# Kernel tuning notes

Measured on AMD Instinct MI355X. Metric: run time of the kernel, lower is better.

## Reference

```python
import jax, jax.numpy as jnp
import numpy as np

DIM = 64  # per-head dim; temperature init = sqrt(DIM)
B, H, S, D = 4, 12, 2048, 64


def setup_inputs() -> dict:
    key = jax.random.key(0)
    kq, kk, kv = jax.random.split(key, 3)
    Q = jax.random.normal(kq, (B, H, S, D), dtype=jnp.float32)
    K = jax.random.normal(kk, (B, H, S, D), dtype=jnp.float32)
    V = jax.random.normal(kv, (B, H, S, D), dtype=jnp.float32)
    temperature = jnp.ones((1,), dtype=jnp.float32) * (DIM ** 0.5)
    return {"Q": Q, "K": K, "V": V, "temperature": temperature}


def reference(Q, K, V, temperature):
    # scores: [B,H,S,S]
    scores = jnp.einsum("bhqd,bhkd->bhqk", Q, K) / temperature
    s = scores.shape[-1]
    eye = jnp.eye(s, dtype=bool)  # diagonal self-exclusion
    scores = jnp.where(eye, -jnp.inf, scores)
    attn = jax.nn.softmax(scores, axis=-1)
    return jnp.einsum("bhqk,bhkd->bhqd", attn, V)
```

## Files before the change

kernel.cpp:

```cpp
#include <hip/hip_runtime.h>
#include <hip/hip_bf16.h>

#define S_LEN 2048
#define D_DIM 64
#define NHEADS 48
#define QT 128
#define KT 64
#define NKT (S_LEN / KT)
#define HEAD_ELEMS ((size_t)S_LEN * D_DIM)
#define WS_NEED (3ull * NHEADS * S_LEN * D_DIM * 2ull)

typedef short bf16x8 __attribute__((ext_vector_type(8)));
typedef float f32x4 __attribute__((ext_vector_type(4)));

__device__ __forceinline__ unsigned short f2bf(float x) {
    unsigned u = __builtin_bit_cast(unsigned, x);
    u = (u + 0x7fffu + ((u >> 16) & 1u)) >> 16;
    return (unsigned short)u;
}

__device__ __forceinline__ unsigned cvtpk(float lo, float hi) {
    unsigned r;
    asm("v_cvt_pk_bf16_f32 %0, %1, %2" : "=v"(r) : "v"(lo), "v"(hi));
    return r;
}

__device__ __forceinline__ void gload16(const void* g, void* l) {
    __builtin_amdgcn_global_load_lds(
        (const __attribute__((address_space(1))) unsigned int*)g,
        (__attribute__((address_space(3))) unsigned int*)l, 16, 0, 0);
}

__global__ __launch_bounds__(256) void lsa_prep(
    const float* __restrict__ Qg, const float* __restrict__ Kg,
    const float* __restrict__ Vg, const float* __restrict__ Tg,
    unsigned short* __restrict__ Qs, unsigned short* __restrict__ Kf,
    unsigned short* __restrict__ Vf) {
    const int b   = blockIdx.x;
    const int tid = threadIdx.x;
    const int r   = tid >> 4;
    const int c4  = (tid & 15) * 4;

    __shared__ __align__(16) unsigned short Kl[4096];
    __shared__ __align__(16) unsigned short Vl[4096];

    const size_t ibase = (size_t)b * 4096;
    const float qscale = 1.442695041f / Tg[0];

#pragma unroll
    for (int it = 0; it < 4; ++it) {
        const int rr = it * 16 + r;
        const size_t off = ibase + (size_t)rr * D_DIM + c4;

        float4 q4 = *(const float4*)(Qg + off);
        uint2 qo;
        qo.x = cvtpk(q4.x * qscale, q4.y * qscale);
        qo.y = cvtpk(q4.z * qscale, q4.w * qscale);
        *(uint2*)&Qs[off] = qo;

        float4 k4 = *(const float4*)(Kg + off);
        {
            const int f = rr >> 4, l15 = rr & 15;
            const int c = c4 >> 5, lhi = (c4 >> 3) & 3, j0 = c4 & 7;
            uint2 ko;
            ko.x = cvtpk(k4.x, k4.y);
            ko.y = cvtpk(k4.z, k4.w);
            *(uint2*)&Kl[c * 2048 + f * 512 + ((lhi << 4) | l15) * 8 + j0] = ko;
        }

        float4 v4 = *(const float4*)(Vg + off);
        {
            const int cc = rr >> 5, rem = rr & 31;
            const int jv = ((rem >> 4) << 2) | (rem & 3);
            const int lhiv = (rem >> 2) & 3;
            const int g = c4 >> 4;
            const int base = cc * 2048 + g * 512 + (lhiv << 7) + jv;
            Vl[base + ((c4 + 0) & 15) * 8] = f2bf(v4.x);
            Vl[base + ((c4 + 1) & 15) * 8] = f2bf(v4.y);
            Vl[base + ((c4 + 2) & 15) * 8] = f2bf(v4.z);
            Vl[base + ((c4 + 3) & 15) * 8] = f2bf(v4.w);
        }
    }
    __syncthreads();
    const uint4* ks = (const uint4*)Kl;
    const uint4* vs = (const uint4*)Vl;
    uint4* kd = (uint4*)(Kf + ibase);
    uint4* vd = (uint4*)(Vf + ibase);
    kd[tid]       = ks[tid];
    kd[tid + 256] = ks[tid + 256];
    vd[tid]       = vs[tid];
    vd[tid + 256] = vs[tid + 256];
}

__global__ __launch_bounds__(256, 2) void lsa_attn_lds(
    const unsigned short* __restrict__ Qs, const unsigned short* __restrict__ Kf,
    const unsigned short* __restrict__ Vf, float* __restrict__ Og) {

    const int bid  = blockIdx.x;
    const int xcd  = bid & 7;
    const int idx  = bid >> 3;
    const int bh   = xcd * 6 + (idx >> 4);
    const int qt   = idx & 15;
    const int tid  = threadIdx.x;
    const int wid  = tid >> 6;
    const int lane = tid & 63;
    const int l15  = lane & 15;
    const int lhi  = lane >> 4;

    __shared__ __align__(16) unsigned short KV[2][2][KT * D_DIM];

    const unsigned short* Qh = Qs + (size_t)bh * HEAD_ELEMS;
    const char* Kh = (const char*)(Kf + (size_t)bh * HEAD_ELEMS);
    const char* Vh = (const char*)(Vf + (size_t)bh * HEAD_ELEMS);
    float* Ob = Og + (size_t)bh * HEAD_ELEMS;

    const int qbase   = qt * QT + wid * 32;
    const int diag_kt = qbase >> 6;

    bf16x8 qf[2][2];
#pragma unroll
    for (int rb = 0; rb < 2; ++rb) {
#pragma unroll
        for (int c = 0; c < 2; ++c) {
            qf[rb][c] = *(const bf16x8*)(Qh + (size_t)(qbase + rb * 16 + l15) * D_DIM
                                            + c * 32 + lhi * 8);
        }
    }

    const f32x4 zero4 = {0.f, 0.f, 0.f, 0.f};
    f32x4 acc[2][4];
    float mrow[2], lp[2];
#pragma unroll
    for (int rb = 0; rb < 2; ++rb) {
#pragma unroll
        for (int g = 0; g < 4; ++g) acc[rb][g] = zero4;
        mrow[rb] = -1e30f; lp[rb] = 0.f;
    }

    bf16x8 vr[8];
    f32x4 sf[2][4];
    bf16x8 pb[2][2];

#define ISSUE(BUF, T) do {                                                     \
    const char* ks_ = Kh + (size_t)(T) * 8192 + wid * 2048;                    \
    const char* vs_ = Vh + (size_t)(T) * 8192 + wid * 2048;                    \
    char* lk_ = (char*)&KV[BUF][0][0] + wid * 2048;                            \
    char* lv_ = (char*)&KV[BUF][1][0] + wid * 2048;                            \
    gload16(ks_ + lane * 16, lk_);                                             \
    gload16(ks_ + 1024 + lane * 16, lk_ + 1024);                               \
    gload16(vs_ + lane * 16, lv_);                                             \
    gload16(vs_ + 1024 + lane * 16, lv_ + 1024);                               \
} while (0)

#define DSQK(BUF) do {                                                         \
    const char* lk_ = (const char*)&KV[BUF][0][0] + lane * 16;                 \
    _Pragma("unroll")                                                          \
    for (int rb = 0; rb < 2; ++rb) {                                           \
        _Pragma("unroll")                                                      \
        for (int f = 0; f < 4; ++f) sf[rb][f] = zero4;                         \
    }                                                                          \
    _Pragma("unroll")                                                          \
    for (int c = 0; c < 2; ++c) {                                              \
        bf16x8 kb_[4];                                                         \
        _Pragma("unroll")                                                      \
        for (int f = 0; f < 4; ++f) {                                          \
            kb_[f] = *(const bf16x8*)(lk_ + c * 4096 + f * 1024);              \
        }                                                                      \
        __builtin_amdgcn_s_setprio(1);                                         \
        _Pragma("unroll")                                                      \
        for (int rb = 0; rb < 2; ++rb) {                                       \
            _Pragma("unroll")                                                  \
            for (int f = 0; f < 4; ++f) {                                      \
                sf[rb][f] = __builtin_amdgcn_mfma_f32_16x16x32_bf16(           \
                    kb_[f], qf[rb][c], sf[rb][f], 0, 0, 0);                    \
            }                                                                  \
        }                                                                      \
        __builtin_amdgcn_s_setprio(0);                                         \
    }                                                                          \
} while (0)

#define DSV(BUF) do {                                                          \
    const char* lv_ = (const char*)&KV[BUF][1][0] + lane * 16;                 \
    _Pragma("unroll")                                                          \
    for (int u = 0; u < 8; ++u) {                                              \
        vr[u] = *(const bf16x8*)(lv_ + (u >> 2) * 4096 + (u & 3) * 1024);      \
    }                                                                          \
} while (0)

#define PV() do {                                                              \
    __builtin_amdgcn_s_setprio(1);                                             \
    _Pragma("unroll")                                                          \
    for (int cc = 0; cc < 2; ++cc) {                                           \
        _Pragma("unroll")                                                      \
        for (int rb = 0; rb < 2; ++rb) {                                       \
            _Pragma("unroll")                                                  \
            for (int g = 0; g < 4; ++g) {                                      \
                acc[rb][g] = __builtin_amdgcn_mfma_f32_16x16x32_bf16(          \
                    vr[cc * 4 + g], pb[rb][cc], acc[rb][g], 0, 0, 0);          \
            }                                                                  \
        }                                                                      \
    }                                                                          \
    __builtin_amdgcn_s_setprio(0);                                             \
} while (0)

#define SMX(T) do {                                                            \
    if ((T) == diag_kt) {                                                      \
        _Pragma("unroll")                                                      \
        for (int rb = 0; rb < 2; ++rb) {                                       \
            const int q_ = qbase + rb * 16 + l15;                              \
            _Pragma("unroll")                                                  \
            for (int f = 0; f < 4; ++f) {                                      \
                _Pragma("unroll")                                              \
                for (int i = 0; i < 4; ++i) {                                  \
                    const int k_ = (T) * KT + f * 16 + lhi * 4 + i;            \
                    if (q_ == k_) sf[rb][f][i] = -1e30f;                       \
                }                                                              \
            }                                                                  \
        }                                                                      \
    }                                                                          \
    _Pragma("unroll")                                                          \
    for (int rb = 0; rb < 2; ++rb) {                                           \
        f32x4 mv_;                                                             \
        _Pragma("unroll")                                                      \
        for (int i = 0; i < 4; ++i) {                                          \
            mv_[i] = fmaxf(fmaxf(sf[rb][0][i], sf[rb][1][i]),                  \
                           fmaxf(sf[rb][2][i], sf[rb][3][i]));                 \
        }                                                                      \
        const float pm_ = fmaxf(fmaxf(mv_[0], mv_[1]), fmaxf(mv_[2], mv_[3]));  \
        if (__any(pm_ > mrow[rb] + 8.0f)) {                                    \
            float m0_ = pm_;                                                   \
            m0_ = fmaxf(m0_, __shfl_xor(m0_, 16));                             \
            m0_ = fmaxf(m0_, __shfl_xor(m0_, 32));                             \
            const float mnew_ = fmaxf(mrow[rb], m0_);                          \
            const float al_ = __builtin_amdgcn_exp2f(mrow[rb] - mnew_);        \
            mrow[rb] = mnew_;                                                  \
            lp[rb] *= al_;                                                     \
            _Pragma("unroll")                                                  \
            for (int g = 0; g < 4; ++g) acc[rb][g] *= al_;                     \
        }                                                                      \
        f32x4 ps_ = zero4;                                                     \
        _Pragma("unroll")                                                      \
        for (int f = 0; f < 4; ++f) {                                          \
            _Pragma("unroll")                                                  \
            for (int i = 0; i < 4; ++i) {                                      \
                sf[rb][f][i] = __builtin_amdgcn_exp2f(sf[rb][f][i] - mrow[rb]); \
            }                                                                  \
            ps_ += sf[rb][f];                                                  \
        }                                                                      \
        lp[rb] += (ps_[0] + ps_[1]) + (ps_[2] + ps_[3]);                       \
        _Pragma("unroll")                                                      \
        for (int cc = 0; cc < 2; ++cc) {                                       \
            uint4 u_;                                                          \
            u_.x = cvtpk(sf[rb][cc * 2][0],     sf[rb][cc * 2][1]);            \
            u_.y = cvtpk(sf[rb][cc * 2][2],     sf[rb][cc * 2][3]);            \
            u_.z = cvtpk(sf[rb][cc * 2 + 1][0], sf[rb][cc * 2 + 1][1]);        \
            u_.w = cvtpk(sf[rb][cc * 2 + 1][2], sf[rb][cc * 2 + 1][3]);        \
            pb[rb][cc] = __builtin_bit_cast(bf16x8, u_);                       \
        }                                                                      \
    }                                                                          \
} while (0)

    ISSUE(0, 0);
    __syncthreads();
    ISSUE(1, 1);
    DSQK(0);
    DSV(0);

#pragma unroll 1
    for (int t = 0; t < NKT - 1; ++t) {
        SMX(t);
        PV();
        __syncthreads();
        if (t + 2 < NKT) ISSUE(t & 1, t + 2);
        DSQK((t + 1) & 1);
        DSV((t + 1) & 1);
    }
    SMX(NKT - 1);
    PV();

#undef ISSUE
#undef DSQK
#undef DSV
#undef PV
#undef SMX

#pragma unroll
    for (int rb = 0; rb < 2; ++rb) {
        float l = lp[rb];
        l += __shfl_xor(l, 16);
        l += __shfl_xor(l, 32);
        const float invl = 1.0f / l;
        const int q = qbase + rb * 16 + l15;
#pragma unroll
        for (int g = 0; g < 4; ++g) {
            float4 o;
            o.x = acc[rb][g][0] * invl;
            o.y = acc[rb][g][1] * invl;
            o.z = acc[rb][g][2] * invl;
            o.w = acc[rb][g][3] * invl;
            *(float4*)(Ob + (size_t)q * D_DIM + g * 16 + lhi * 4) = o;
        }
    }
}

__device__ __forceinline__ int swzK_fb(int row, int col) {
    return (row << 6) + (col ^ ((row & 7) << 3));
}
__device__ __forceinline__ int swzV_fb(int row, int col) {
    int f = (row ^ (row >> 3)) & 7;
    return (row << 6) + (col ^ (f << 3));
}

__global__ __launch_bounds__(256, 2) void lsa_attn_fb(
    const float* __restrict__ Qg, const float* __restrict__ Kg,
    const float* __restrict__ Vg, const float* __restrict__ Tg,
    float* __restrict__ Og) {

    const int bid  = blockIdx.x;
    const int bh   = bid >> 4;
    const int qt   = bid & 15;
    const int tid  = threadIdx.x;
    const int wid  = tid >> 6;
    const int lane = tid & 63;
    const int l15  = lane & 15;
    const int lhi  = lane >> 4;

    __shared__ __align__(16) unsigned short Kt[64 * D_DIM];
    __shared__ __align__(16) unsigned short Vt[D_DIM * 64];

    const size_t base = (size_t)bh * HEAD_ELEMS;
    const float* Qb = Qg + base;
    const float* Kb = Kg + base;
    const float* Vb = Vg + base;
    float*       Ob = Og + base;

    const float inv_t = 1.0f / Tg[0];
    const int qbase = qt * QT + wid * 32;
    const int diag_kt = qbase >> 6;

    bf16x8 qf[2][2];
#pragma unroll
    for (int rb = 0; rb < 2; ++rb) {
#pragma unroll
        for (int c = 0; c < 2; ++c) {
            const float* src = Qb + (size_t)(qbase + rb * 16 + l15) * D_DIM + c * 32 + lhi * 8;
            float4 a = *(const float4*)(src);
            float4 b = *(const float4*)(src + 4);
            bf16x8 v;
            v[0] = (short)f2bf(a.x * inv_t); v[1] = (short)f2bf(a.y * inv_t);
            v[2] = (short)f2bf(a.z * inv_t); v[3] = (short)f2bf(a.w * inv_t);
            v[4] = (short)f2bf(b.x * inv_t); v[5] = (short)f2bf(b.y * inv_t);
            v[6] = (short)f2bf(b.z * inv_t); v[7] = (short)f2bf(b.w * inv_t);
            qf[rb][c] = v;
        }
    }

    const f32x4 zero4 = {0.f, 0.f, 0.f, 0.f};
    f32x4 acc[2][4];
    float mrow[2], lrow[2];
#pragma unroll
    for (int rb = 0; rb < 2; ++rb) {
#pragma unroll
        for (int g = 0; g < 4; ++g) acc[rb][g] = zero4;
        mrow[rb] = -1e30f; lrow[rb] = 0.f;
    }

    const int ld_r = tid >> 4;
    const int ld_c = (tid & 15) * 4;
    float4 kreg[4], vreg[4];

#define LOAD_TILE(KT_IDX) do {                                                 \
    const int kb0_ = (KT_IDX) * 64;                                            \
    _Pragma("unroll")                                                          \
    for (int it = 0; it < 4; ++it) {                                           \
        const int r_ = it * 16 + ld_r;                                         \
        kreg[it] = *(const float4*)(Kb + (size_t)(kb0_ + r_) * D_DIM + ld_c);  \
        vreg[it] = *(const float4*)(Vb + (size_t)(kb0_ + r_) * D_DIM + ld_c);  \
    }                                                                          \
} while (0)

    LOAD_TILE(0);

    for (int kt = 0; kt < 32; ++kt) {
        const int kb0 = kt * 64;
        __syncthreads();
#pragma unroll
        for (int it = 0; it < 4; ++it) {
            const int r = it * 16 + ld_r;
            unsigned lo = (unsigned)f2bf(kreg[it].x) | ((unsigned)f2bf(kreg[it].y) << 16);
            unsigned hi = (unsigned)f2bf(kreg[it].z) | ((unsigned)f2bf(kreg[it].w) << 16);
            *(uint2*)&Kt[swzK_fb(r, ld_c)] = make_uint2(lo, hi);
            Vt[swzV_fb(ld_c + 0, r)] = f2bf(vreg[it].x);
            Vt[swzV_fb(ld_c + 1, r)] = f2bf(vreg[it].y);
            Vt[swzV_fb(ld_c + 2, r)] = f2bf(vreg[it].z);
            Vt[swzV_fb(ld_c + 3, r)] = f2bf(vreg[it].w);
        }
        __syncthreads();
        if (kt + 1 < 32) LOAD_TILE(kt + 1);

        f32x4 sf[2][4];
#pragma unroll
        for (int rb = 0; rb < 2; ++rb) {
#pragma unroll
            for (int f = 0; f < 4; ++f) sf[rb][f] = zero4;
        }

#pragma unroll
        for (int c = 0; c < 2; ++c) {
            bf16x8 kb[4];
#pragma unroll
            for (int f = 0; f < 4; ++f)
                kb[f] = *(const bf16x8*)&Kt[swzK_fb(f * 16 + l15, c * 32 + lhi * 8)];
#pragma unroll
            for (int rb = 0; rb < 2; ++rb) {
#pragma unroll
                for (int f = 0; f < 4; ++f)
                    sf[rb][f] = __builtin_amdgcn_mfma_f32_16x16x32_bf16(
                        kb[f], qf[rb][c], sf[rb][f], 0, 0, 0);
            }
        }

        if (kt == diag_kt) {
#pragma unroll
            for (int rb = 0; rb < 2; ++rb) {
                const int q = qbase + rb * 16 + l15;
#pragma unroll
                for (int f = 0; f < 4; ++f) {
#pragma unroll
                    for (int i = 0; i < 4; ++i) {
                        const int k = kb0 + f * 16 + lhi * 4 + i;
                        if (q == k) sf[rb][f][i] = -1e30f;
                    }
                }
            }
        }

        bf16x8 pb[2][2];
#pragma unroll
        for (int rb = 0; rb < 2; ++rb) {
            f32x4 mv;
#pragma unroll
            for (int i = 0; i < 4; ++i)
                mv[i] = fmaxf(fmaxf(sf[rb][0][i], sf[rb][1][i]),
                              fmaxf(sf[rb][2][i], sf[rb][3][i]));
            float m0 = fmaxf(fmaxf(mv[0], mv[1]), fmaxf(mv[2], mv[3]));
            m0 = fmaxf(m0, __shfl_xor(m0, 16));
            m0 = fmaxf(m0, __shfl_xor(m0, 32));
            const float mnew  = fmaxf(mrow[rb], m0);
            const float alpha = __expf(mrow[rb] - mnew);
            mrow[rb] = mnew;
            f32x4 ps = zero4;
#pragma unroll
            for (int f = 0; f < 4; ++f) {
#pragma unroll
                for (int i = 0; i < 4; ++i)
                    sf[rb][f][i] = __expf(sf[rb][f][i] - mnew);
                ps += sf[rb][f];
            }
            float s0 = (ps[0] + ps[1]) + (ps[2] + ps[3]);
            s0 += __shfl_xor(s0, 16);
            s0 += __shfl_xor(s0, 32);
            lrow[rb] = lrow[rb] * alpha + s0;
#pragma unroll
            for (int g = 0; g < 4; ++g) acc[rb][g] *= alpha;
#pragma unroll
            for (int cc = 0; cc < 2; ++cc) {
                bf16x8 v;
#pragma unroll
                for (int j = 0; j < 8; ++j)
                    v[j] = (short)f2bf(sf[rb][cc * 2 + (j >> 2)][j & 3]);
                pb[rb][cc] = v;
            }
        }

#pragma unroll
        for (int cc = 0; cc < 2; ++cc) {
            bf16x8 va[4];
#pragma unroll
            for (int g = 0; g < 4; ++g) {
                const int row = g * 16 + l15;
                uint2 lo = *(const uint2*)&Vt[swzV_fb(row, cc * 32 + lhi * 4)];
                uint2 hi = *(const uint2*)&Vt[swzV_fb(row, cc * 32 + 16 + lhi * 4)];
                bf16x8 t;
                ((uint2*)&t)[0] = lo;
                ((uint2*)&t)[1] = hi;
                va[g] = t;
            }
#pragma unroll
            for (int rb = 0; rb < 2; ++rb) {
#pragma unroll
                for (int g = 0; g < 4; ++g)
                    acc[rb][g] = __builtin_amdgcn_mfma_f32_16x16x32_bf16(
                        va[g], pb[rb][cc], acc[rb][g], 0, 0, 0);
            }
        }
    }
#undef LOAD_TILE

#pragma unroll
    for (int rb = 0; rb < 2; ++rb) {
        const float invl = 1.0f / lrow[rb];
        const int q = qbase + rb * 16 + l15;
#pragma unroll
        for (int g = 0; g < 4; ++g) {
            float4 o;
            o.x = acc[rb][g][0] * invl;
            o.y = acc[rb][g][1] * invl;
            o.z = acc[rb][g][2] * invl;
            o.w = acc[rb][g][3] * invl;
            *(float4*)(Ob + (size_t)q * D_DIM + g * 16 + lhi * 4) = o;
        }
    }
}

extern "C" void kernel_launch(void* const* d_in, const int* in_sizes, int n_in,
                              void* d_out, int out_size, void* d_ws, size_t ws_size,
                              hipStream_t stream) {
    const float* Q = (const float*)d_in[0];
    const float* K = (const float*)d_in[1];
    const float* V = (const float*)d_in[2];
    const float* T = (const float*)d_in[3];
    float* O = (float*)d_out;

    if (ws_size >= WS_NEED) {
        unsigned short* Qs = (unsigned short*)d_ws;
        unsigned short* Kf = Qs + NHEADS * HEAD_ELEMS;
        unsigned short* Vf = Kf + NHEADS * HEAD_ELEMS;
        hipLaunchKernelGGL(lsa_prep, dim3(NHEADS * NKT), dim3(256), 0, stream,
                           Q, K, V, T, Qs, Kf, Vf);
        hipLaunchKernelGGL(lsa_attn_lds, dim3(NHEADS * (S_LEN / QT)), dim3(256), 0, stream,
                           Qs, Kf, Vf, O);
    } else {
        hipLaunchKernelGGL(lsa_attn_fb, dim3(NHEADS * (S_LEN / QT)), dim3(256), 0, stream,
                           Q, K, V, T, O);
    }
}
```

Before: 87.74 us.

## Split query tile across eight waves with sixteen rows each

The attention kernel now launches 512 threads per block, with each of eight waves handling 16 query rows instead of four waves handling 32. K/V tile loads are split across the eight waves. The aim is more waves in flight and fewer registers per wave to hide latency. In exchange, each K/V tile read from LDS is reused across half as many rows per wave, so LDS read traffic relative to MFMA work doubles, and block-wide syncs now involve more waves.

```diff
diff --git a/kernel.cpp b/kernel.cpp
--- a/kernel.cpp
+++ b/kernel.cpp
@@ -92,7 +92,7 @@
     vd[tid + 256] = vs[tid + 256];
 }
 
-__global__ __launch_bounds__(256, 2) void lsa_attn_lds(
+__global__ __launch_bounds__(512, 6) void lsa_attn_w8(
     const unsigned short* __restrict__ Qs, const unsigned short* __restrict__ Kf,
     const unsigned short* __restrict__ Vf, float* __restrict__ Og) {
 
@@ -114,51 +114,39 @@
     const char* Vh = (const char*)(Vf + (size_t)bh * HEAD_ELEMS);
     float* Ob = Og + (size_t)bh * HEAD_ELEMS;
 
-    const int qbase   = qt * QT + wid * 32;
+    const int qbase   = qt * QT + wid * 16;
     const int diag_kt = qbase >> 6;
 
-    bf16x8 qf[2][2];
-#pragma unroll
-    for (int rb = 0; rb < 2; ++rb) {
-#pragma unroll
-        for (int c = 0; c < 2; ++c) {
-            qf[rb][c] = *(const bf16x8*)(Qh + (size_t)(qbase + rb * 16 + l15) * D_DIM
-                                            + c * 32 + lhi * 8);
-        }
+    bf16x8 qf[2];
+#pragma unroll
+    for (int c = 0; c < 2; ++c) {
+        qf[c] = *(const bf16x8*)(Qh + (size_t)(qbase + l15) * D_DIM + c * 32 + lhi * 8);
     }
 
     const f32x4 zero4 = {0.f, 0.f, 0.f, 0.f};
-    f32x4 acc[2][4];
-    float mrow[2], lp[2];
-#pragma unroll
-    for (int rb = 0; rb < 2; ++rb) {
-#pragma unroll
-        for (int g = 0; g < 4; ++g) acc[rb][g] = zero4;
-        mrow[rb] = -1e30f; lp[rb] = 0.f;
-    }
+    f32x4 acc[4];
+    float mrow, lp;
+#pragma unroll
+    for (int g = 0; g < 4; ++g) acc[g] = zero4;
+    mrow = -1e30f; lp = 0.f;
 
     bf16x8 vr[8];
-    f32x4 sf[2][4];
-    bf16x8 pb[2][2];
+    f32x4 sf[4];
+    bf16x8 pb[2];
 
 #define ISSUE(BUF, T) do {                                                     \
-    const char* ks_ = Kh + (size_t)(T) * 8192 + wid * 2048;                    \
-    const char* vs_ = Vh + (size_t)(T) * 8192 + wid * 2048;                    \
-    char* lk_ = (char*)&KV[BUF][0][0] + wid * 2048;                            \
-    char* lv_ = (char*)&KV[BUF][1][0] + wid * 2048;                            \
+    const char* ks_ = Kh + (size_t)(T) * 8192 + wid * 1024;                    \
+    const char* vs_ = Vh + (size_t)(T) * 8192 + wid * 1024;                    \
+    char* lk_ = (char*)&KV[BUF][0][0] + wid * 1024;                            \
+    char* lv_ = (char*)&KV[BUF][1][0] + wid * 1024;                            \
     gload16(ks_ + lane * 16, lk_);                                             \
-    gload16(ks_ + 1024 + lane * 16, lk_ + 1024);                               \
     gload16(vs_ + lane * 16, lv_);                                             \
-    gload16(vs_ + 1024 + lane * 16, lv_ + 1024);                               \
 } while (0)
 
 #define DSQK(BUF) do {                                                         \
     const char* lk_ = (const char*)&KV[BUF][0][0] + lane * 16;                 \
     _Pragma("unroll")                                                          \
-    for (int rb = 0; rb < 2; ++rb) {                                           \
-        _Pragma("unroll")                                                      \
-        for (int f = 0; f < 4; ++f) sf[rb][f] = zero4;                         \
-    }                                                                          \
+    for (int f = 0; f < 4; ++f) sf[f] = zero4;                                 \
     _Pragma("unroll")                                                          \
     for (int c = 0; c < 2; ++c) {                                              \
         bf16x8 kb_[4];                                                         \
@@ -168,12 +156,9 @@
         }                                                                      \
         __builtin_amdgcn_s_setprio(1);                                         \
         _Pragma("unroll")                                                      \
-        for (int rb = 0; rb < 2; ++rb) {                                       \
-            _Pragma("unroll")                                                  \
-            for (int f = 0; f < 4; ++f) {                                      \
-                sf[rb][f] = __builtin_amdgcn_mfma_f32_16x16x32_bf16(           \
-                    kb_[f], qf[rb][c], sf[rb][f], 0, 0, 0);                    \
-            }                                                                  \
+        for (int f = 0; f < 4; ++f) {                                          \
+            sf[f] = __builtin_amdgcn_mfma_f32_16x16x32_bf16(                   \
+                kb_[f], qf[c], sf[f], 0, 0, 0);                                \
         }                                                                      \
         __builtin_amdgcn_s_setprio(0);                                         \
     }                                                                          \
@@ -192,12 +177,9 @@
     _Pragma("unroll")                                                          \
     for (int cc = 0; cc < 2; ++cc) {                                           \
         _Pragma("unroll")                                                      \
-        for (int rb = 0; rb < 2; ++rb) {                                       \
-            _Pragma("unroll")                                                  \
-            for (int g = 0; g < 4; ++g) {                                      \
-                acc[rb][g] = __builtin_amdgcn_mfma_f32_16x16x32_bf16(          \
-                    vr[cc * 4 + g], pb[rb][cc], acc[rb][g], 0, 0, 0);          \
-            }                                                                  \
+        for (int g = 0; g < 4; ++g) {                                          \
+            acc[g] = __builtin_amdgcn_mfma_f32_16x16x32_bf16(                  \
+                vr[cc * 4 + g], pb[cc], acc[g], 0, 0, 0);                      \
         }                                                                      \
     }                                                                          \
     __builtin_amdgcn_s_setprio(0);                                             \
@@ -205,57 +187,53 @@
 
 #define SMX(T) do {                                                            \
     if ((T) == diag_kt) {                                                      \
-        _Pragma("unroll")                                                      \
-        for (int rb = 0; rb < 2; ++rb) {                                       \
-            const int q_ = qbase + rb * 16 + l15;                              \
+        const int q_ = qbase + l15;                                            \
+        _Pragma("unroll")                                                      \
+        for (int f = 0; f < 4; ++f) {                                          \
             _Pragma("unroll")                                                  \
-            for (int f = 0; f < 4; ++f) {                                      \
-                _Pragma("unroll")                                              \
-                for (int i = 0; i < 4; ++i) {                                  \
-                    const int k_ = (T) * KT + f * 16 + lhi * 4 + i;            \
-                    if (q_ == k_) sf[rb][f][i] = -1e30f;                       \
-                }                                                              \
+            for (int i = 0; i < 4; ++i) {                                      \
+                const int k_ = (T) * KT + f * 16 + lhi * 4 + i;                \
+                if (q_ == k_) sf[f][i] = -1e30f;                               \
             }                                                                  \
         }                                                                      \
     }                                                                          \
-    _Pragma("unroll")                                                          \
-    for (int rb = 0; rb < 2; ++rb) {                                           \
+    {                                                                          \
         f32x4 mv_;                                                             \
         _Pragma("unroll")                                                      \
         for (int i = 0; i < 4; ++i) {                                          \
-            mv_[i] = fmaxf(fmaxf(sf[rb][0][i], sf[rb][1][i]),                  \
-                           fmaxf(sf[rb][2][i], sf[rb][3][i]));                 \
-        }                                                                      \
-        const float pm_ = fmaxf(fmaxf(mv_[0], mv_[1]), fmaxf(mv_[2], mv_[3]));  \
-        if (__any(pm_ > mrow[rb] + 8.0f)) {                                    \
+            mv_[i] = fmaxf(fmaxf(sf[0][i], sf[1][i]),                          \
+                           fmaxf(sf[2][i], sf[3][i]));                         \
+        }                                                                      \
+        const float pm_ = fmaxf(fmaxf(mv_[0], mv_[1]), fmaxf(mv_[2], mv_[3])); \
+        if (__any(pm_ > mrow + 8.0f)) {                                        \
             float m0_ = pm_;                                                   \
             m0_ = fmaxf(m0_, __shfl_xor(m0_, 16));                             \
             m0_ = fmaxf(m0_, __shfl_xor(m0_, 32));                             \
-            const float mnew_ = fmaxf(mrow[rb], m0_);                          \
-            const float al_ = __builtin_amdgcn_exp2f(mrow[rb] - mnew_);        \
-            mrow[rb] = mnew_;                                                  \
-            lp[rb] *= al_;                                                     \
+            const float mnew_ = fmaxf(mrow, m0_);                              \
+            const float al_ = __builtin_amdgcn_exp2f(mrow - mnew_);            \
+            mrow = mnew_;                                                      \
+            lp *= al_;                                                         \
             _Pragma("unroll")                                                  \
-            for (int g = 0; g < 4; ++g) acc[rb][g] *= al_;                     \
+            for (int g = 0; g < 4; ++g) acc[g] *= al_;                         \
         }                                                                      \
         f32x4 ps_ = zero4;                                                     \
         _Pragma("unroll")                                                      \
         for (int f = 0; f < 4; ++f) {                                          \
             _Pragma("unroll")                                                  \
             for (int i = 0; i < 4; ++i) {                                      \
-                sf[rb][f][i] = __builtin_amdgcn_exp2f(sf[rb][f][i] - mrow[rb]); \
+                sf[f][i] = __builtin_amdgcn_exp2f(sf[f][i] - mrow);            \
             }                                                                  \
-            ps_ += sf[rb][f];                                                  \
-        }                                                                      \
-        lp[rb] += (ps_[0] + ps_[1]) + (ps_[2] + ps_[3]);                       \
+            ps_ += sf[f];                                                      \
+        }                                                                      \
+        lp += (ps_[0] + ps_[1]) + (ps_[2] + ps_[3]);                           \
         _Pragma("unroll")                                                      \
         for (int cc = 0; cc < 2; ++cc) {                                       \
             uint4 u_;                                                          \
-            u_.x = cvtpk(sf[rb][cc * 2][0],     sf[rb][cc * 2][1]);            \
-            u_.y = cvtpk(sf[rb][cc * 2][2],     sf[rb][cc * 2][3]);            \
-            u_.z = cvtpk(sf[rb][cc * 2 + 1][0], sf[rb][cc * 2 + 1][1]);        \
-            u_.w = cvtpk(sf[rb][cc * 2 + 1][2], sf[rb][cc * 2 + 1][3]);        \
-            pb[rb][cc] = __builtin_bit_cast(bf16x8, u_);                       \
+            u_.x = cvtpk(sf[cc * 2][0],     sf[cc * 2][1]);                    \
+            u_.y = cvtpk(sf[cc * 2][2],     sf[cc * 2][3]);                    \
+            u_.z = cvtpk(sf[cc * 2 + 1][0], sf[cc * 2 + 1][1]);                \
+            u_.w = cvtpk(sf[cc * 2 + 1][2], sf[cc * 2 + 1][3]);                \
+            pb[cc] = __builtin_bit_cast(bf16x8, u_);                           \
         }                                                                      \
     }                                                                          \
 } while (0)
@@ -284,20 +262,19 @@
 #undef PV
 #undef SMX
 
-#pragma unroll
-    for (int rb = 0; rb < 2; ++rb) {
-        float l = lp[rb];
+    {
+        float l = lp;
         l += __shfl_xor(l, 16);
         l += __shfl_xor(l, 32);
         const float invl = 1.0f / l;
-        const int q = qbase + rb * 16 + l15;
+        const int q = qbase + l15;
 #pragma unroll
         for (int g = 0; g < 4; ++g) {
             float4 o;
-            o.x = acc[rb][g][0] * invl;
-            o.y = acc[rb][g][1] * invl;
-            o.z = acc[rb][g][2] * invl;
-            o.w = acc[rb][g][3] * invl;
+            o.x = acc[g][0] * invl;
+            o.y = acc[g][1] * invl;
+            o.z = acc[g][2] * invl;
+            o.w = acc[g][3] * invl;
             *(float4*)(Ob + (size_t)q * D_DIM + g * 16 + lhi * 4) = o;
         }
     }
@@ -528,7 +505,7 @@
         unsigned short* Vf = Kf + NHEADS * HEAD_ELEMS;
         hipLaunchKernelGGL(lsa_prep, dim3(NHEADS * NKT), dim3(256), 0, stream,
                            Q, K, V, T, Qs, Kf, Vf);
-        hipLaunchKernelGGL(lsa_attn_lds, dim3(NHEADS * (S_LEN / QT)), dim3(256), 0, stream,
+        hipLaunchKernelGGL(lsa_attn_w8, dim3(NHEADS * (S_LEN / QT)), dim3(512), 0, stream,
                            Qs, Kf, Vf, O);
     } else {
         hipLaunchKernelGGL(lsa_attn_fb, dim3(NHEADS * (S_LEN / QT)), dim3(256), 0, stream,
```

New measurement: 154.1 us. +75.6%, slower.

## Software-pipeline QK^T of next tile with softmax of current tile

Applied to the files above, without the earlier changes.

Restructures the attention main loop into a two-tile unrolled pipeline with two score register sets. The QK^T MFMAs for tile t+1 are issued before the softmax and PV of tile t, so matrix-core work overlaps the exp and reduction work. The next tile's global-to-LDS load is issued right after the barrier. The cost is a second 2x4 f32x4 score array held live in registers, which may pressure occupancy at two blocks per CU or cause spills.

```diff
diff --git a/kernel.cpp b/kernel.cpp
--- a/kernel.cpp
+++ b/kernel.cpp
@@ -92,7 +92,7 @@
     vd[tid + 256] = vs[tid + 256];
 }
 
-__global__ __launch_bounds__(256, 2) void lsa_attn_lds(
+__global__ __launch_bounds__(256, 2) void lsa_attn_db(
     const unsigned short* __restrict__ Qs, const unsigned short* __restrict__ Kf,
     const unsigned short* __restrict__ Vf, float* __restrict__ Og) {
 
@@ -138,26 +138,26 @@
     }
 
     bf16x8 vr[8];
-    f32x4 sf[2][4];
+    f32x4 sfA[2][4], sfB[2][4];
     bf16x8 pb[2][2];
 
-#define ISSUE(BUF, T) do {                                                     \
+#define ISSUE(T) do {                                                          \
     const char* ks_ = Kh + (size_t)(T) * 8192 + wid * 2048;                    \
     const char* vs_ = Vh + (size_t)(T) * 8192 + wid * 2048;                    \
-    char* lk_ = (char*)&KV[BUF][0][0] + wid * 2048;                            \
-    char* lv_ = (char*)&KV[BUF][1][0] + wid * 2048;                            \
+    char* lk_ = (char*)&KV[(T) & 1][0][0] + wid * 2048;                        \
+    char* lv_ = (char*)&KV[(T) & 1][1][0] + wid * 2048;                        \
     gload16(ks_ + lane * 16, lk_);                                             \
     gload16(ks_ + 1024 + lane * 16, lk_ + 1024);                               \
     gload16(vs_ + lane * 16, lv_);                                             \
     gload16(vs_ + 1024 + lane * 16, lv_ + 1024);                               \
 } while (0)
 
-#define DSQK(BUF) do {                                                         \
-    const char* lk_ = (const char*)&KV[BUF][0][0] + lane * 16;                 \
+#define DSQK(T, SF) do {                                                       \
+    const char* lk_ = (const char*)&KV[(T) & 1][0][0] + lane * 16;             \
     _Pragma("unroll")                                                          \
     for (int rb = 0; rb < 2; ++rb) {                                           \
         _Pragma("unroll")                                                      \
-        for (int f = 0; f < 4; ++f) sf[rb][f] = zero4;                         \
+        for (int f = 0; f < 4; ++f) SF[rb][f] = zero4;                         \
     }                                                                          \
     _Pragma("unroll")                                                          \
     for (int c = 0; c < 2; ++c) {                                              \
@@ -171,16 +171,16 @@
         for (int rb = 0; rb < 2; ++rb) {                                       \
             _Pragma("unroll")                                                  \
             for (int f = 0; f < 4; ++f) {                                      \
-                sf[rb][f] = __builtin_amdgcn_mfma_f32_16x16x32_bf16(           \
-                    kb_[f], qf[rb][c], sf[rb][f], 0, 0, 0);                    \
+                SF[rb][f] = __builtin_amdgcn_mfma_f32_16x16x32_bf16(           \
+                    kb_[f], qf[rb][c], SF[rb][f], 0, 0, 0);                    \
             }                                                                  \
         }                                                                      \
         __builtin_amdgcn_s_setprio(0);                                         \
     }                                                                          \
 } while (0)
 
-#define DSV(BUF) do {                                                          \
-    const char* lv_ = (const char*)&KV[BUF][1][0] + lane * 16;                 \
+#define DSV(T) do {                                                            \
+    const char* lv_ = (const char*)&KV[(T) & 1][1][0] + lane * 16;             \
     _Pragma("unroll")                                                          \
     for (int u = 0; u < 8; ++u) {                                              \
         vr[u] = *(const bf16x8*)(lv_ + (u >> 2) * 4096 + (u & 3) * 1024);      \
@@ -203,7 +203,7 @@
     __builtin_amdgcn_s_setprio(0);                                             \
 } while (0)
 
-#define SMX(T) do {                                                            \
+#define SMX(T, SF) do {                                                        \
     if ((T) == diag_kt) {                                                      \
         _Pragma("unroll")                                                      \
         for (int rb = 0; rb < 2; ++rb) {                                       \
@@ -213,7 +213,7 @@
                 _Pragma("unroll")                                              \
                 for (int i = 0; i < 4; ++i) {                                  \
                     const int k_ = (T) * KT + f * 16 + lhi * 4 + i;            \
-                    if (q_ == k_) sf[rb][f][i] = -1e30f;                       \
+                    if (q_ == k_) SF[rb][f][i] = -1e30f;                       \
                 }                                                              \
             }                                                                  \
         }                                                                      \
@@ -223,8 +223,8 @@
         f32x4 mv_;                                                             \
         _Pragma("unroll")                                                      \
         for (int i = 0; i < 4; ++i) {                                          \
-            mv_[i] = fmaxf(fmaxf(sf[rb][0][i], sf[rb][1][i]),                  \
-                           fmaxf(sf[rb][2][i], sf[rb][3][i]));                 \
+            mv_[i] = fmaxf(fmaxf(SF[rb][0][i], SF[rb][1][i]),                  \
+                           fmaxf(SF[rb][2][i], SF[rb][3][i]));                 \
         }                                                                      \
         const float pm_ = fmaxf(fmaxf(mv_[0], mv_[1]), fmaxf(mv_[2], mv_[3]));  \
         if (__any(pm_ > mrow[rb] + 8.0f)) {                                    \
@@ -243,39 +243,50 @@
         for (int f = 0; f < 4; ++f) {                                          \
             _Pragma("unroll")                                                  \
             for (int i = 0; i < 4; ++i) {                                      \
-                sf[rb][f][i] = __builtin_amdgcn_exp2f(sf[rb][f][i] - mrow[rb]); \
+                SF[rb][f][i] = __builtin_amdgcn_exp2f(SF[rb][f][i] - mrow[rb]); \
             }                                                                  \
-            ps_ += sf[rb][f];                                                  \
+            ps_ += SF[rb][f];                                                  \
         }                                                                      \
         lp[rb] += (ps_[0] + ps_[1]) + (ps_[2] + ps_[3]);                       \
         _Pragma("unroll")                                                      \
         for (int cc = 0; cc < 2; ++cc) {                                       \
             uint4 u_;                                                          \
-            u_.x = cvtpk(sf[rb][cc * 2][0],     sf[rb][cc * 2][1]);            \
-            u_.y = cvtpk(sf[rb][cc * 2][2],     sf[rb][cc * 2][3]);            \
-            u_.z = cvtpk(sf[rb][cc * 2 + 1][0], sf[rb][cc * 2 + 1][1]);        \
-            u_.w = cvtpk(sf[rb][cc * 2 + 1][2], sf[rb][cc * 2 + 1][3]);        \
+            u_.x = cvtpk(SF[rb][cc * 2][0],     SF[rb][cc * 2][1]);            \
+            u_.y = cvtpk(SF[rb][cc * 2][2],     SF[rb][cc * 2][3]);            \
+            u_.z = cvtpk(SF[rb][cc * 2 + 1][0], SF[rb][cc * 2 + 1][1]);        \
+            u_.w = cvtpk(SF[rb][cc * 2 + 1][2], SF[rb][cc * 2 + 1][3]);        \
             pb[rb][cc] = __builtin_bit_cast(bf16x8, u_);                       \
         }                                                                      \
     }                                                                          \
 } while (0)
 
-    ISSUE(0, 0);
+    ISSUE(0);
     __syncthreads();
-    ISSUE(1, 1);
-    DSQK(0);
+    ISSUE(1);
+    DSQK(0, sfA);
     DSV(0);
 
 #pragma unroll 1
-    for (int t = 0; t < NKT - 1; ++t) {
-        SMX(t);
+    for (int t = 0; t < NKT - 2; t += 2) {
+        __syncthreads();
+        ISSUE(t + 2);
+        DSQK(t + 1, sfB);
+        SMX(t, sfA);
         PV();
+        DSV(t + 1);
         __syncthreads();
-        if (t + 2 < NKT) ISSUE(t & 1, t + 2);
-        DSQK((t + 1) & 1);
-        DSV((t + 1) & 1);
-    }
-    SMX(NKT - 1);
+        ISSUE(t + 3);
+        DSQK(t + 2, sfA);
+        SMX(t + 1, sfB);
+        PV();
+        DSV(t + 2);
+    }
+    __syncthreads();
+    DSQK(NKT - 1, sfB);
+    SMX(NKT - 2, sfA);
+    PV();
+    DSV(NKT - 1);
+    SMX(NKT - 1, sfB);
     PV();
 
 #undef ISSUE
@@ -528,7 +539,7 @@
         unsigned short* Vf = Kf + NHEADS * HEAD_ELEMS;
         hipLaunchKernelGGL(lsa_prep, dim3(NHEADS * NKT), dim3(256), 0, stream,
                            Q, K, V, T, Qs, Kf, Vf);
-        hipLaunchKernelGGL(lsa_attn_lds, dim3(NHEADS * (S_LEN / QT)), dim3(256), 0, stream,
+        hipLaunchKernelGGL(lsa_attn_db, dim3(NHEADS * (S_LEN / QT)), dim3(256), 0, stream,
                            Qs, Kf, Vf, O);
     } else {
         hipLaunchKernelGGL(lsa_attn_fb, dim3(NHEADS * (S_LEN / QT)), dim3(256), 0, stream,
```

Result: no change. 89.44 us (+1.9%).

## Fold Q conversion into attention kernel and use lazy max rescaling softmax

Applied to the files above, without the earlier changes.

Q is now loaded as fp32 and scaled/converted to bf16 directly in the attention kernel, removing the Q pass from the prep kernel and its workspace buffer. After the first key tile, the online softmax no longer computes a running max per tile. It exponentiates against the stale max and rescales only when any row's partial sum exceeds a threshold. This removes the per-tile cross-lane max reductions and accumulator rescales, but it can overflow if a later tile's scores exceed the stored max by a large margin.

```diff
diff --git a/kernel.cpp b/kernel.cpp
--- a/kernel.cpp
+++ b/kernel.cpp
@@ -8,7 +8,7 @@
 #define KT 64
 #define NKT (S_LEN / KT)
 #define HEAD_ELEMS ((size_t)S_LEN * D_DIM)
-#define WS_NEED (3ull * NHEADS * S_LEN * D_DIM * 2ull)
+#define WS_NEED (2ull * NHEADS * S_LEN * D_DIM * 2ull)
 
 typedef short bf16x8 __attribute__((ext_vector_type(8)));
 typedef float f32x4 __attribute__((ext_vector_type(4)));
@@ -32,10 +32,8 @@
 }
 
 __global__ __launch_bounds__(256) void lsa_prep(
-    const float* __restrict__ Qg, const float* __restrict__ Kg,
-    const float* __restrict__ Vg, const float* __restrict__ Tg,
-    unsigned short* __restrict__ Qs, unsigned short* __restrict__ Kf,
-    unsigned short* __restrict__ Vf) {
+    const float* __restrict__ Kg, const float* __restrict__ Vg,
+    unsigned short* __restrict__ Kf, unsigned short* __restrict__ Vf) {
     const int b   = blockIdx.x;
     const int tid = threadIdx.x;
     const int r   = tid >> 4;
@@ -45,18 +43,11 @@
     __shared__ __align__(16) unsigned short Vl[4096];
 
     const size_t ibase = (size_t)b * 4096;
-    const float qscale = 1.442695041f / Tg[0];
 
 #pragma unroll
     for (int it = 0; it < 4; ++it) {
         const int rr = it * 16 + r;
         const size_t off = ibase + (size_t)rr * D_DIM + c4;
-
-        float4 q4 = *(const float4*)(Qg + off);
-        uint2 qo;
-        qo.x = cvtpk(q4.x * qscale, q4.y * qscale);
-        qo.y = cvtpk(q4.z * qscale, q4.w * qscale);
-        *(uint2*)&Qs[off] = qo;
 
         float4 k4 = *(const float4*)(Kg + off);
         {
@@ -92,9 +83,10 @@
     vd[tid + 256] = vs[tid + 256];
 }
 
-__global__ __launch_bounds__(256, 2) void lsa_attn_lds(
-    const unsigned short* __restrict__ Qs, const unsigned short* __restrict__ Kf,
-    const unsigned short* __restrict__ Vf, float* __restrict__ Og) {
+__global__ __launch_bounds__(256, 2) void lsa_attn_f(
+    const float* __restrict__ Qg, const float* __restrict__ Tg,
+    const unsigned short* __restrict__ Kf, const unsigned short* __restrict__ Vf,
+    float* __restrict__ Og) {
 
     const int bid  = blockIdx.x;
     const int xcd  = bid & 7;
@@ -109,21 +101,30 @@
 
     __shared__ __align__(16) unsigned short KV[2][2][KT * D_DIM];
 
-    const unsigned short* Qh = Qs + (size_t)bh * HEAD_ELEMS;
+    const float* Qb = Qg + (size_t)bh * HEAD_ELEMS;
     const char* Kh = (const char*)(Kf + (size_t)bh * HEAD_ELEMS);
     const char* Vh = (const char*)(Vf + (size_t)bh * HEAD_ELEMS);
     float* Ob = Og + (size_t)bh * HEAD_ELEMS;
 
     const int qbase   = qt * QT + wid * 32;
     const int diag_kt = qbase >> 6;
+    const float qscale = 1.442695041f / Tg[0];
 
     bf16x8 qf[2][2];
 #pragma unroll
     for (int rb = 0; rb < 2; ++rb) {
 #pragma unroll
         for (int c = 0; c < 2; ++c) {
-            qf[rb][c] = *(const bf16x8*)(Qh + (size_t)(qbase + rb * 16 + l15) * D_DIM
-                                            + c * 32 + lhi * 8);
+            const float* src = Qb + (size_t)(qbase + rb * 16 + l15) * D_DIM
+                                  + c * 32 + lhi * 8;
+            float4 a = *(const float4*)(src);
+            float4 b = *(const float4*)(src + 4);
+            uint4 u;
+            u.x = cvtpk(a.x * qscale, a.y * qscale);
+            u.y = cvtpk(a.z * qscale, a.w * qscale);
+            u.z = cvtpk(b.x * qscale, b.y * qscale);
+            u.w = cvtpk(b.z * qscale, b.w * qscale);
+            qf[rb][c] = __builtin_bit_cast(bf16x8, u);
         }
     }
 
@@ -203,7 +204,7 @@
     __builtin_amdgcn_s_setprio(0);                                             \
 } while (0)
 
-#define SMX(T) do {                                                            \
+#define DIAG(T) do {                                                           \
     if ((T) == diag_kt) {                                                      \
         _Pragma("unroll")                                                      \
         for (int rb = 0; rb < 2; ++rb) {                                       \
@@ -218,6 +219,22 @@
             }                                                                  \
         }                                                                      \
     }                                                                          \
+} while (0)
+
+#define PACK(rb) do {                                                          \
+    _Pragma("unroll")                                                          \
+    for (int cc = 0; cc < 2; ++cc) {                                           \
+        uint4 u_;                                                              \
+        u_.x = cvtpk(sf[rb][cc * 2][0],     sf[rb][cc * 2][1]);                \
+        u_.y = cvtpk(sf[rb][cc * 2][2],     sf[rb][cc * 2][3]);                \
+        u_.z = cvtpk(sf[rb][cc * 2 + 1][0], sf[rb][cc * 2 + 1][1]);            \
+        u_.w = cvtpk(sf[rb][cc * 2 + 1][2], sf[rb][cc * 2 + 1][3]);            \
+        pb[rb][cc] = __builtin_bit_cast(bf16x8, u_);                           \
+    }                                                                          \
+} while (0)
+
+#define SM_FULL(T) do {                                                        \
+    DIAG(T);                                                                   \
     _Pragma("unroll")                                                          \
     for (int rb = 0; rb < 2; ++rb) {                                           \
         f32x4 mv_;                                                             \
@@ -248,15 +265,50 @@
             ps_ += sf[rb][f];                                                  \
         }                                                                      \
         lp[rb] += (ps_[0] + ps_[1]) + (ps_[2] + ps_[3]);                       \
-        _Pragma("unroll")                                                      \
-        for (int cc = 0; cc < 2; ++cc) {                                       \
-            uint4 u_;                                                          \
-            u_.x = cvtpk(sf[rb][cc * 2][0],     sf[rb][cc * 2][1]);            \
-            u_.y = cvtpk(sf[rb][cc * 2][2],     sf[rb][cc * 2][3]);            \
-            u_.z = cvtpk(sf[rb][cc * 2 + 1][0], sf[rb][cc * 2 + 1][1]);        \
-            u_.w = cvtpk(sf[rb][cc * 2 + 1][2], sf[rb][cc * 2 + 1][3]);        \
-            pb[rb][cc] = __builtin_bit_cast(bf16x8, u_);                       \
-        }                                                                      \
+        PACK(rb);                                                              \
+    }                                                                          \
+} while (0)
+
+#define SM_FAST(T) do {                                                        \
+    DIAG(T);                                                                   \
+    _Pragma("unroll")                                                          \
+    for (int rb = 0; rb < 2; ++rb) {                                           \
+        f32x4 ps_ = zero4;                                                     \
+        _Pragma("unroll")                                                      \
+        for (int f = 0; f < 4; ++f) {                                          \
+            _Pragma("unroll")                                                  \
+            for (int i = 0; i < 4; ++i) {                                      \
+                sf[rb][f][i] = __builtin_amdgcn_exp2f(sf[rb][f][i] - mrow[rb]); \
+            }                                                                  \
+            ps_ += sf[rb][f];                                                  \
+        }                                                                      \
+        const float s0_ = (ps_[0] + ps_[1]) + (ps_[2] + ps_[3]);               \
+        if (__any(s0_ > 256.0f)) {                                             \
+            f32x4 mv_;                                                         \
+            _Pragma("unroll")                                                  \
+            for (int i = 0; i < 4; ++i) {                                      \
+                mv_[i] = fmaxf(fmaxf(sf[rb][0][i], sf[rb][1][i]),              \
+                               fmaxf(sf[rb][2][i], sf[rb][3][i]));             \
+            }                                                                  \
+            float mx_ = fmaxf(fmaxf(mv_[0], mv_[1]), fmaxf(mv_[2], mv_[3]));    \
+            mx_ = fmaxf(mx_, __shfl_xor(mx_, 16));                             \
+            mx_ = fmaxf(mx_, __shfl_xor(mx_, 32));                             \
+            mx_ = fmaxf(mx_, 1.0f);                                            \
+            const float L_  = __log2f(mx_);                                    \
+            const float al_ = __builtin_amdgcn_exp2f(-L_);                     \
+            mrow[rb] += L_;                                                    \
+            _Pragma("unroll")                                                  \
+            for (int f = 0; f < 4; ++f) {                                      \
+                _Pragma("unroll")                                              \
+                for (int i = 0; i < 4; ++i) sf[rb][f][i] *= al_;               \
+            }                                                                  \
+            _Pragma("unroll")                                                  \
+            for (int g = 0; g < 4; ++g) acc[rb][g] *= al_;                     \
+            lp[rb] = (lp[rb] + s0_) * al_;                                     \
+        } else {                                                               \
+            lp[rb] += s0_;                                                     \
+        }                                                                      \
+        PACK(rb);                                                              \
     }                                                                          \
 } while (0)
 
@@ -268,21 +320,24 @@
 
 #pragma unroll 1
     for (int t = 0; t < NKT - 1; ++t) {
-        SMX(t);
+        if (t == 0) { SM_FULL(0); } else { SM_FAST(t); }
         PV();
         __syncthreads();
         if (t + 2 < NKT) ISSUE(t & 1, t + 2);
         DSQK((t + 1) & 1);
         DSV((t + 1) & 1);
     }
-    SMX(NKT - 1);
+    SM_FAST(NKT - 1);
     PV();
 
 #undef ISSUE
 #undef DSQK
 #undef DSV
 #undef PV
-#undef SMX
+#undef DIAG
+#undef PACK
+#undef SM_FULL
+#undef SM_FAST
 
 #pragma unroll
     for (int rb = 0; rb < 2; ++rb) {
@@ -523,13 +578,12 @@
     float* O = (float*)d_out;
 
     if (ws_size >= WS_NEED) {
-        unsigned short* Qs = (unsigned short*)d_ws;
-        unsigned short* Kf = Qs + NHEADS * HEAD_ELEMS;
+        unsigned short* Kf = (unsigned short*)d_ws;
         unsigned short* Vf = Kf + NHEADS * HEAD_ELEMS;
         hipLaunchKernelGGL(lsa_prep, dim3(NHEADS * NKT), dim3(256), 0, stream,
-                           Q, K, V, T, Qs, Kf, Vf);
-        hipLaunchKernelGGL(lsa_attn_lds, dim3(NHEADS * (S_LEN / QT)), dim3(256), 0, stream,
-                           Qs, Kf, Vf, O);
+                           K, V, Kf, Vf);
+        hipLaunchKernelGGL(lsa_attn_f, dim3(NHEADS * (S_LEN / QT)), dim3(256), 0, stream,
+                           Q, T, Kf, Vf, O);
     } else {
         hipLaunchKernelGGL(lsa_attn_fb, dim3(NHEADS * (S_LEN / QT)), dim3(256), 0, stream,
                            Q, K, V, T, O);
```

New measurement: 90.67 us. +3.3%, slower.
